# Kernel optimization log

Measured on AMD Instinct MI355X. Metric: run time of the kernel, lower is better.

Reference implementation:

```python
import jax, jax.numpy as jnp
import numpy as np

N = 50000      # nodes per graph
E = 1_600_000  # edges per graph (before self-loops)
D = 128        # node feature dim
H = 9          # attention heads
C = 8          # channels per head
HC = H * C     # 72
NEG_SLOPE = 0.2


def setup_inputs() -> dict:
    key = jax.random.key(0)
    ks = iter(jax.random.split(key, 32))
    inp = {}
    for i in (1, 2, 3):
        inp[f"x{i}"] = jax.random.normal(next(ks), (N, D), dtype=jnp.float32)
        inp[f"edge_index{i}"] = jax.random.randint(next(ks), (2, E), 0, N, dtype=jnp.int64)
        inp[f"W{i}"] = jax.random.normal(next(ks), (D, HC), dtype=jnp.float32) * (1.0 / np.sqrt(D))
        inp[f"att_src{i}"] = jax.random.normal(next(ks), (H, C), dtype=jnp.float32) * 0.1
        inp[f"att_dst{i}"] = jax.random.normal(next(ks), (H, C), dtype=jnp.float32) * 0.1
        inp[f"b{i}"] = jnp.zeros((HC,), dtype=jnp.float32)
    inp["fnn_W"] = jax.random.normal(next(ks), (3 * HC, 2), dtype=jnp.float32) * (1.0 / np.sqrt(3 * HC))
    inp["fnn_b"] = jnp.zeros((2,), dtype=jnp.float32)
    return inp


def gat_conv(x, edge_index, W, att_src, att_dst, bias):
    """PyG GATConv (eval mode): linear -> per-edge LeakyReLU score -> edge softmax
    over incoming edges per dst node -> scatter-add aggregate. Self-loops added."""
    n = x.shape[0]
    loop = jnp.arange(n, dtype=edge_index.dtype)
    src = jnp.concatenate([edge_index[0], loop])  # [E+N]
    dst = jnp.concatenate([edge_index[1], loop])
    h = (x @ W).reshape(n, H, C)                  # [N,H,C]
    a_s = jnp.einsum('nhc,hc->nh', h, att_src)    # [N,H]
    a_d = jnp.einsum('nhc,hc->nh', h, att_dst)
    alpha = jax.nn.leaky_relu(a_s[src] + a_d[dst], NEG_SLOPE)   # [E+N,H]
    m = jax.ops.segment_max(alpha, dst, num_segments=n)         # stable softmax per dst
    alpha = jnp.exp(alpha - m[dst])
    denom = jax.ops.segment_sum(alpha, dst, num_segments=n)
    alpha = alpha / (denom[dst] + 1e-16)
    out = jax.ops.segment_sum(h[src] * alpha[:, :, None], dst, num_segments=n)
    return out.reshape(n, HC) + bias


def reference(x1, x2, x3, edge_index1, edge_index2, edge_index3,
              W1, att_src1, att_dst1, b1,
              W2, att_src2, att_dst2, b2,
              W3, att_src3, att_dst3, b3,
              fnn_W, fnn_b):
    o1 = gat_conv(x1, edge_index1, W1, att_src1, att_dst1, b1)
    o2 = gat_conv(x2, edge_index2, W2, att_src2, att_dst2, b2)
    o3 = gat_conv(x3, edge_index3, W3, att_src3, att_dst3, b3)
    x = jax.nn.relu(jnp.concatenate([o1, o2, o3], axis=1))  # [N, 216]
    logits = x @ fnn_W + fnn_b                              # [N, 2]
    return jax.nn.softmax(logits, axis=1)
```

## Files before the change

kernel.cpp:

```cpp
#include <hip/hip_runtime.h>
#include <hip/hip_fp16.h>

#define NN 50000
#define NE 1600000
#define DD 128
#define NH 9
#define NC 8
#define HCH 72
#define NEG 0.2f
#define NBUCK 196
#define NSEG 16
#define SPAD 17
#define EPB 16
#define BCH (256*EPB)
#define BSTRIDE 10240
#define BCSTRIDE 16
#define GEMMB2 ((NN + 63) / 64)
#define BINB ((NE + BCH - 1) / BCH)
#define WTP 136
#define CLP 88

typedef _Float16 f16x8 __attribute__((ext_vector_type(8)));
typedef float f32x4 __attribute__((ext_vector_type(4)));

__device__ __forceinline__ unsigned short f2h(float f) {
  return __half_as_ushort(__float2half_rn(f));
}
__device__ __forceinline__ float h2f(unsigned short u) {
  return __half2float(__ushort_as_half(u));
}
__device__ __forceinline__ float hlo(unsigned u) {
  return __half2float(__ushort_as_half((unsigned short)(u & 0xFFFFu)));
}
__device__ __forceinline__ float hhi(unsigned u) {
  return __half2float(__ushort_as_half((unsigned short)(u >> 16)));
}

struct GP {
  const float* x; const int* ei; const float* W;
  const float* as; const float* ad; const float* b;
  uint4* h2;
  unsigned short* as2;
  float* a_d; float* out;
  int* offs2;
  int* bcursor;
  unsigned int* pairs;
  int* csr;
};
struct GT { GP g[3]; };

__global__ __launch_bounds__(256) void k_gemm_bin(GT t) {
  const GP G = t.g[blockIdx.z];
  __shared__ __align__(16) char smem[80 * WTP * 2 + 64 * CLP * 2];
  const int tid = threadIdx.x;

  if (blockIdx.x >= GEMMB2) {
    int* lh    = (int*)smem;
    int* lbase = lh + 256;
    int* lcur  = lbase + 256;
    const int e0 = (blockIdx.x - GEMMB2) * BCH;
    for (int i = tid; i < NBUCK; i += 256) lh[i] = 0;
    __syncthreads();
    int dsts[EPB], srcs[EPB];
    #pragma unroll
    for (int k = 0; k < EPB; ++k) {
      const int e = e0 + k * 256 + tid;
      if (e < NE) {
        dsts[k] = G.ei[NE + e];
        srcs[k] = G.ei[e];
        atomicAdd(&lh[dsts[k] >> 8], 1);
      } else dsts[k] = -1;
    }
    __syncthreads();
    for (int i = tid; i < NBUCK; i += 256) {
      int c = lh[i];
      lbase[i] = c ? atomicAdd(&G.bcursor[i * BCSTRIDE], c) : 0;
      lcur[i] = 0;
    }
    __syncthreads();
    #pragma unroll
    for (int k = 0; k < EPB; ++k) {
      if (dsts[k] >= 0) {
        int b = dsts[k] >> 8;
        int pos = lbase[b] + atomicAdd(&lcur[b], 1);
        if (pos < BSTRIDE)
          G.pairs[(size_t)b * BSTRIDE + pos] =
              (unsigned)srcs[k] | ((unsigned)(dsts[k] & 255) << 16);
      }
    }
    return;
  }

  _Float16* Wt = (_Float16*)smem;
  _Float16* Cl = (_Float16*)(smem + 80 * WTP * 2);

  for (int i = tid; i < DD * 80; i += 256) {
    const int k = i / 80;
    const int c = i - k * 80;
    const float v = (c < HCH) ? G.W[k * HCH + c] : 0.f;
    Wt[c * WTP + k] = (_Float16)v;
  }
  __syncthreads();

  const int wv = tid >> 6;
  const int ln = tid & 63;
  const int rl = ln & 15;
  const int kg = ln >> 4;
  const int n0 = blockIdx.x << 6;
  int arow = n0 + wv * 16 + rl;
  if (arow >= NN) arow = NN - 1;
  const float4* xr = (const float4*)(G.x + (size_t)arow * DD) + (kg << 1);

  f32x4 acc[5];
  #pragma unroll
  for (int ct = 0; ct < 5; ++ct) acc[ct] = (f32x4){0.f, 0.f, 0.f, 0.f};

  #pragma unroll
  for (int ks = 0; ks < 4; ++ks) {
    const float4 xa = xr[ks * 8];
    const float4 xb = xr[ks * 8 + 1];
    float xs[8] = {xa.x, xa.y, xa.z, xa.w, xb.x, xb.y, xb.z, xb.w};
    f16x8 ahi, alo;
    #pragma unroll
    for (int j = 0; j < 8; ++j) {
      const _Float16 h = (_Float16)xs[j];
      ahi[j] = h;
      alo[j] = (_Float16)(xs[j] - (float)h);
    }
    const int kb = ks * 32 + kg * 8;
    #pragma unroll
    for (int ct = 0; ct < 5; ++ct) {
      const f16x8 bf = *(const f16x8*)&Wt[(ct * 16 + rl) * WTP + kb];
      acc[ct] = __builtin_amdgcn_mfma_f32_16x16x32_f16(ahi, bf, acc[ct], 0, 0, 0);
      acc[ct] = __builtin_amdgcn_mfma_f32_16x16x32_f16(alo, bf, acc[ct], 0, 0, 0);
    }
  }

  #pragma unroll
  for (int ct = 0; ct < 5; ++ct) {
    #pragma unroll
    for (int j = 0; j < 4; ++j)
      Cl[(wv * 16 + kg * 4 + j) * CLP + ct * 16 + rl] = (_Float16)acc[ct][j];
  }
  __syncthreads();

  for (int p = tid; p < 64 * NH; p += 256) {
    const int node = p / NH;
    const int hd = p - node * NH;
    const int n = n0 + node;
    if (n >= NN) continue;
    const uint4 hv = *(const uint4*)&Cl[node * CLP + hd * NC];
    const float h0 = hlo(hv.x), h1 = hhi(hv.x), h2v = hlo(hv.y), h3 = hhi(hv.y);
    const float h4 = hlo(hv.z), h5 = hhi(hv.z), h6 = hlo(hv.w), h7 = hhi(hv.w);
    const float4 As0 = *(const float4*)(G.as + hd * NC);
    const float4 As1 = *(const float4*)(G.as + hd * NC + 4);
    const float4 Ad0 = *(const float4*)(G.ad + hd * NC);
    const float4 Ad1 = *(const float4*)(G.ad + hd * NC + 4);
    const float ssrc = h0 * As0.x + h1 * As0.y + h2v * As0.z + h3 * As0.w
                     + h4 * As1.x + h5 * As1.y + h6 * As1.z + h7 * As1.w;
    const float sdst = h0 * Ad0.x + h1 * Ad0.y + h2v * Ad0.z + h3 * Ad0.w
                     + h4 * Ad1.x + h5 * Ad1.y + h6 * Ad1.z + h7 * Ad1.w;
    G.h2[(size_t)n * NH + hd] = hv;
    G.as2[n * NH + hd] = f2h(ssrc);
    G.a_d[n * NH + hd] = sdst;
  }
}

__global__ __launch_bounds__(256) void k_scat2(GT t) {
  const GP G = t.g[blockIdx.z];
  const int b = blockIdx.x;
  const int d0 = b << 8;
  __shared__ int cnt[256 * SPAD];
  __shared__ int ssum[256];
  const int tid = threadIdx.x;
  const int estart = b * BSTRIDE;
  const int eend = estart + G.bcursor[b * BCSTRIDE];
  for (int i = tid; i < 256 * SPAD; i += 256) cnt[i] = 0;
  __syncthreads();
  for (int e = estart + tid; e < eend; e += 256) {
    unsigned p = G.pairs[e];
    int key = (int)((p >> 16) * SPAD + ((p & 0xFFFFu) >> 12));
    atomicAdd(&cnt[key], 1);
  }
  __syncthreads();
  int local[NSEG];
  int sum = 0;
  #pragma unroll
  for (int i = 0; i < NSEG; ++i) { local[i] = sum; sum += cnt[tid * SPAD + i]; }
  ssum[tid] = sum;
  __syncthreads();
  int run = sum;
  for (int off = 1; off < 256; off <<= 1) {
    int u = (tid >= off) ? ssum[tid - off] : 0;
    __syncthreads();
    run += u;
    ssum[tid] = run;
    __syncthreads();
  }
  const int texcl = run - sum;
  int* o2 = G.offs2 + ((size_t)d0 << 4);
  #pragma unroll
  for (int i = 0; i < NSEG; ++i) {
    int v = estart + texcl + local[i];
    cnt[tid * SPAD + i] = v;
    o2[tid * NSEG + i] = v;
  }
  __syncthreads();
  for (int e = estart + tid; e < eend; e += 256) {
    unsigned p = G.pairs[e];
    int key = (int)((p >> 16) * SPAD + ((p & 0xFFFFu) >> 12));
    int pos = atomicAdd(&cnt[key], 1);
    G.csr[pos] = (int)(p & 0xFFFFu);
  }
}

__global__ __launch_bounds__(256) void k_agg(GP G) {
  const int gid = blockIdx.x * 256 + threadIdx.x;
  const bool active = (gid < NN * NH);
  int n = 0, head = 0;
  if (active) { n = gid / NH; head = gid - n * NH; }
  float denom = 0.f;
  float4 acc0 = make_float4(0.f, 0.f, 0.f, 0.f);
  float4 acc1 = make_float4(0.f, 0.f, 0.f, 0.f);
  float ad_n = 0.f;
  int gb[5] = {0, 0, 0, 0, 0};
  if (active) {
    ad_n = G.a_d[n * NH + head];
    const int* o2 = G.offs2 + ((size_t)n << 4);
    gb[0] = o2[0]; gb[1] = o2[4]; gb[2] = o2[8]; gb[3] = o2[12]; gb[4] = o2[13];
    float sl = h2f(G.as2[n * NH + head]) + ad_n;
    sl = (sl > 0.f) ? sl : NEG * sl;
    float wl = __expf(sl);
    uint4 hs = G.h2[(size_t)n * NH + head];
    denom = wl;
    acc0.x = wl * hlo(hs.x); acc0.y = wl * hhi(hs.x);
    acc0.z = wl * hlo(hs.y); acc0.w = wl * hhi(hs.y);
    acc1.x = wl * hlo(hs.z); acc1.y = wl * hhi(hs.z);
    acc1.z = wl * hlo(hs.w); acc1.w = wl * hhi(hs.w);
  }
  #pragma unroll
  for (int g = 0; g < 4; ++g) {
    int e = gb[g];
    const int en = gb[g + 1];
    for (; e + 4 <= en; e += 4) {
      int s0 = G.csr[e];
      int s1 = G.csr[e + 1];
      int s2 = G.csr[e + 2];
      int s3 = G.csr[e + 3];
      unsigned short u0 = G.as2[s0 * NH + head];
      unsigned short u1 = G.as2[s1 * NH + head];
      unsigned short u2 = G.as2[s2 * NH + head];
      unsigned short u3 = G.as2[s3 * NH + head];
      uint4 v0 = G.h2[(size_t)s0 * NH + head];
      uint4 v1 = G.h2[(size_t)s1 * NH + head];
      uint4 v2 = G.h2[(size_t)s2 * NH + head];
      uint4 v3 = G.h2[(size_t)s3 * NH + head];
      float t0 = h2f(u0) + ad_n;
      float t1 = h2f(u1) + ad_n;
      float t2 = h2f(u2) + ad_n;
      float t3 = h2f(u3) + ad_n;
      t0 = (t0 > 0.f) ? t0 : NEG * t0;
      t1 = (t1 > 0.f) ? t1 : NEG * t1;
      t2 = (t2 > 0.f) ? t2 : NEG * t2;
      t3 = (t3 > 0.f) ? t3 : NEG * t3;
      float w0 = __expf(t0);
      float w1 = __expf(t1);
      float w2 = __expf(t2);
      float w3 = __expf(t3);
      denom += (w0 + w1) + (w2 + w3);
      acc0.x = fmaf(w0, hlo(v0.x), acc0.x); acc0.y = fmaf(w0, hhi(v0.x), acc0.y);
      acc0.z = fmaf(w0, hlo(v0.y), acc0.z); acc0.w = fmaf(w0, hhi(v0.y), acc0.w);
      acc1.x = fmaf(w0, hlo(v0.z), acc1.x); acc1.y = fmaf(w0, hhi(v0.z), acc1.y);
      acc1.z = fmaf(w0, hlo(v0.w), acc1.z); acc1.w = fmaf(w0, hhi(v0.w), acc1.w);
      acc0.x = fmaf(w1, hlo(v1.x), acc0.x); acc0.y = fmaf(w1, hhi(v1.x), acc0.y);
      acc0.z = fmaf(w1, hlo(v1.y), acc0.z); acc0.w = fmaf(w1, hhi(v1.y), acc0.w);
      acc1.x = fmaf(w1, hlo(v1.z), acc1.x); acc1.y = fmaf(w1, hhi(v1.z), acc1.y);
      acc1.z = fmaf(w1, hlo(v1.w), acc1.z); acc1.w = fmaf(w1, hhi(v1.w), acc1.w);
      acc0.x = fmaf(w2, hlo(v2.x), acc0.x); acc0.y = fmaf(w2, hhi(v2.x), acc0.y);
      acc0.z = fmaf(w2, hlo(v2.y), acc0.z); acc0.w = fmaf(w2, hhi(v2.y), acc0.w);
      acc1.x = fmaf(w2, hlo(v2.z), acc1.x); acc1.y = fmaf(w2, hhi(v2.z), acc1.y);
      acc1.z = fmaf(w2, hlo(v2.w), acc1.z); acc1.w = fmaf(w2, hhi(v2.w), acc1.w);
      acc0.x = fmaf(w3, hlo(v3.x), acc0.x); acc0.y = fmaf(w3, hhi(v3.x), acc0.y);
      acc0.z = fmaf(w3, hlo(v3.y), acc0.z); acc0.w = fmaf(w3, hhi(v3.y), acc0.w);
      acc1.x = fmaf(w3, hlo(v3.z), acc1.x); acc1.y = fmaf(w3, hhi(v3.z), acc1.y);
      acc1.z = fmaf(w3, hlo(v3.w), acc1.z); acc1.w = fmaf(w3, hhi(v3.w), acc1.w);
    }
    for (; e < en; ++e) {
      int src = G.csr[e];
      float sc = h2f(G.as2[src * NH + head]) + ad_n;
      sc = (sc > 0.f) ? sc : NEG * sc;
      float w = __expf(sc);
      uint4 hv = G.h2[(size_t)src * NH + head];
      denom += w;
      acc0.x = fmaf(w, hlo(hv.x), acc0.x); acc0.y = fmaf(w, hhi(hv.x), acc0.y);
      acc0.z = fmaf(w, hlo(hv.y), acc0.z); acc0.w = fmaf(w, hhi(hv.y), acc0.w);
      acc1.x = fmaf(w, hlo(hv.z), acc1.x); acc1.y = fmaf(w, hhi(hv.z), acc1.y);
      acc1.z = fmaf(w, hlo(hv.w), acc1.z); acc1.w = fmaf(w, hhi(hv.w), acc1.w);
    }
    __syncthreads();
  }
  if (!active) return;
  float inv = 1.f / (denom + 1e-16f);
  const float* bp = G.b + head * NC;
  float4 o0, o1;
  o0.x = acc0.x * inv + bp[0]; o0.y = acc0.y * inv + bp[1];
  o0.z = acc0.z * inv + bp[2]; o0.w = acc0.w * inv + bp[3];
  o1.x = acc1.x * inv + bp[4]; o1.y = acc1.y * inv + bp[5];
  o1.z = acc1.z * inv + bp[6]; o1.w = acc1.w * inv + bp[7];
  float4* op = (float4*)(G.out + (size_t)n * HCH + head * NC);
  op[0] = o0; op[1] = o1;
}

__global__ __launch_bounds__(256) void k_fnn(const float* __restrict__ o1,
                                             const float* __restrict__ o2,
                                             const float* __restrict__ o3,
                                             const float* __restrict__ fw,
                                             const float* __restrict__ fb,
                                             float* __restrict__ out) {
  const int tid = blockIdx.x * 256 + threadIdx.x;
  const int n = tid >> 6;
  const int lane = tid & 63;
  if (n >= NN) return;
  float acc0 = 0.f, acc1 = 0.f;
  for (int j = lane; j < 3 * HCH; j += 64) {
    const int g = j / HCH;
    const int c = j - g * HCH;
    const float* og = (g == 0) ? o1 : (g == 1) ? o2 : o3;
    float v = og[(size_t)n * HCH + c];
    v = v > 0.f ? v : 0.f;
    acc0 = fmaf(v, fw[2 * j], acc0);
    acc1 = fmaf(v, fw[2 * j + 1], acc1);
  }
  #pragma unroll
  for (int off = 32; off > 0; off >>= 1) {
    acc0 += __shfl_down(acc0, off, 64);
    acc1 += __shfl_down(acc1, off, 64);
  }
  if (lane == 0) {
    float l0 = acc0 + fb[0], l1 = acc1 + fb[1];
    float m = fmaxf(l0, l1);
    float e0 = __expf(l0 - m), e1 = __expf(l1 - m);
    float inv = 1.f / (e0 + e1);
    out[(size_t)n * 2] = e0 * inv;
    out[(size_t)n * 2 + 1] = e1 * inv;
  }
}

extern "C" void kernel_launch(void* const* d_in, const int* in_sizes, int n_in,
                              void* d_out, int out_size, void* d_ws, size_t ws_size,
                              hipStream_t stream) {
  (void)in_sizes; (void)n_in; (void)out_size; (void)ws_size;
  GT t;
  char* w = (char*)d_ws;
  size_t off = 0;
  auto carve = [&](size_t bytes) -> void* {
    void* p = w + off;
    off = (off + bytes + 255) & ~(size_t)255;
    return p;
  };
  int* bc_all = (int*)carve(3 * NBUCK * BCSTRIDE * 4);
  for (int g = 0; g < 3; ++g) {
    GP& G = t.g[g];
    G.x  = (const float*)d_in[6 * g + 0];
    G.ei = (const int*)d_in[6 * g + 1];
    G.W  = (const float*)d_in[6 * g + 2];
    G.as = (const float*)d_in[6 * g + 3];
    G.ad = (const float*)d_in[6 * g + 4];
    G.b  = (const float*)d_in[6 * g + 5];
    G.bcursor = bc_all + g * NBUCK * BCSTRIDE;
    G.h2   = (uint4*)carve((size_t)NN * NH * 16);
    G.as2  = (unsigned short*)carve((size_t)NN * NH * 2);
    G.a_d  = (float*)carve((size_t)NN * NH * 4);
    G.out  = (float*)carve((size_t)NN * HCH * 4);
    G.offs2 = (int*)carve((size_t)NBUCK * 256 * NSEG * 4);
    G.pairs = (unsigned int*)carve((size_t)NBUCK * BSTRIDE * 4);
    G.csr   = (int*)carve((size_t)NBUCK * BSTRIDE * 4);
  }
  const float* fw = (const float*)d_in[18];
  const float* fb = (const float*)d_in[19];
  float* outp = (float*)d_out;

  dim3 b256(256, 1, 1);
  hipMemsetAsync(bc_all, 0, 3 * NBUCK * BCSTRIDE * 4, stream);
  k_gemm_bin<<<dim3(GEMMB2 + BINB, 1, 3), b256, 0, stream>>>(t);
  k_scat2   <<<dim3(NBUCK, 1, 3), b256, 0, stream>>>(t);
  for (int g = 0; g < 3; ++g)
    k_agg   <<<dim3((NN * NH + 255) / 256, 1, 1), b256, 0, stream>>>(t.g[g]);
  k_fnn     <<<(NN * 64 + 255) / 256, b256, 0, stream>>>(t.g[0].out, t.g[1].out, t.g[2].out, fw, fb, outp);
}
```

Before: 433.1 us.

## Split binning kernel, stage pairs in LDS for coalesced writes, merge agg launches

Edge binning moves out of the fused gemm/bin kernel into its own kernel. Each block now sorts its edges into buckets locally in shared memory using a prefix scan, then writes contiguous runs to the global pairs array, replacing scattered per-edge global writes. The three per-graph aggregation launches are merged into one grid, which cuts launch overhead and tail idle time. In exchange it adds an extra kernel launch, more LDS use per binning block, and gives up the overlap between GEMM and binning that the fused kernel had.

Measured after the change: 436.8 us. About the same (+0.8%).

```diff
diff --git a/kernel.cpp b/kernel.cpp
--- a/kernel.cpp
+++ b/kernel.cpp
@@ -17,6 +17,7 @@
 #define BCSTRIDE 16
 #define GEMMB2 ((NN + 63) / 64)
 #define BINB ((NE + BCH - 1) / BCH)
+#define AGGB ((NN * NH + 255) / 256)
 #define WTP 136
 #define CLP 88
 
@@ -49,48 +50,10 @@
 };
 struct GT { GP g[3]; };
 
-__global__ __launch_bounds__(256) void k_gemm_bin(GT t) {
+__global__ __launch_bounds__(256) void k_gemm(GT t) {
   const GP G = t.g[blockIdx.z];
   __shared__ __align__(16) char smem[80 * WTP * 2 + 64 * CLP * 2];
   const int tid = threadIdx.x;
-
-  if (blockIdx.x >= GEMMB2) {
-    int* lh    = (int*)smem;
-    int* lbase = lh + 256;
-    int* lcur  = lbase + 256;
-    const int e0 = (blockIdx.x - GEMMB2) * BCH;
-    for (int i = tid; i < NBUCK; i += 256) lh[i] = 0;
-    __syncthreads();
-    int dsts[EPB], srcs[EPB];
-    #pragma unroll
-    for (int k = 0; k < EPB; ++k) {
-      const int e = e0 + k * 256 + tid;
-      if (e < NE) {
-        dsts[k] = G.ei[NE + e];
-        srcs[k] = G.ei[e];
-        atomicAdd(&lh[dsts[k] >> 8], 1);
-      } else dsts[k] = -1;
-    }
-    __syncthreads();
-    for (int i = tid; i < NBUCK; i += 256) {
-      int c = lh[i];
-      lbase[i] = c ? atomicAdd(&G.bcursor[i * BCSTRIDE], c) : 0;
-      lcur[i] = 0;
-    }
-    __syncthreads();
-    #pragma unroll
-    for (int k = 0; k < EPB; ++k) {
-      if (dsts[k] >= 0) {
-        int b = dsts[k] >> 8;
-        int pos = lbase[b] + atomicAdd(&lcur[b], 1);
-        if (pos < BSTRIDE)
-          G.pairs[(size_t)b * BSTRIDE + pos] =
-              (unsigned)srcs[k] | ((unsigned)(dsts[k] & 255) << 16);
-      }
-    }
-    return;
-  }
-
   _Float16* Wt = (_Float16*)smem;
   _Float16* Cl = (_Float16*)(smem + 80 * WTP * 2);
 
@@ -166,6 +129,66 @@
   }
 }
 
+__global__ __launch_bounds__(256) void k_bin(GT t) {
+  const GP G = t.g[blockIdx.z];
+  __shared__ unsigned stage[BCH];
+  __shared__ unsigned char bkt[BCH];
+  __shared__ int hist[NBUCK];
+  __shared__ int gdelta[NBUCK];
+  __shared__ int ssum[256];
+  const int tid = threadIdx.x;
+  const int e0 = blockIdx.x * BCH;
+
+  for (int i = tid; i < NBUCK; i += 256) hist[i] = 0;
+  __syncthreads();
+  int dsts[EPB], srcs[EPB];
+  #pragma unroll
+  for (int k = 0; k < EPB; ++k) {
+    const int e = e0 + k * 256 + tid;
+    if (e < NE) {
+      dsts[k] = G.ei[NE + e];
+      srcs[k] = G.ei[e];
+      atomicAdd(&hist[dsts[k] >> 8], 1);
+    } else dsts[k] = -1;
+  }
+  __syncthreads();
+  const int cnt_t = (tid < NBUCK) ? hist[tid] : 0;
+  ssum[tid] = cnt_t;
+  __syncthreads();
+  int run = cnt_t;
+  for (int off = 1; off < 256; off <<= 1) {
+    int u = (tid >= off) ? ssum[tid - off] : 0;
+    __syncthreads();
+    run += u;
+    ssum[tid] = run;
+    __syncthreads();
+  }
+  const int excl = run - cnt_t;
+  if (tid < NBUCK) {
+    const int gbase = cnt_t ? atomicAdd(&G.bcursor[tid * BCSTRIDE], cnt_t) : 0;
+    gdelta[tid] = tid * BSTRIDE + gbase - excl;
+    hist[tid] = excl;
+  }
+  __syncthreads();
+  #pragma unroll
+  for (int k = 0; k < EPB; ++k) {
+    if (dsts[k] >= 0) {
+      const int b = dsts[k] >> 8;
+      const int pos = atomicAdd(&hist[b], 1);
+      stage[pos] = (unsigned)srcs[k] | ((unsigned)(dsts[k] & 255) << 16);
+      bkt[pos] = (unsigned char)b;
+    }
+  }
+  __syncthreads();
+  const int total = (e0 + BCH <= NE) ? BCH : (NE - e0);
+  for (int i = tid; i < total; i += 256) {
+    const int b = bkt[i];
+    const int addr = gdelta[b] + i;
+    if (addr - b * BSTRIDE < BSTRIDE)
+      G.pairs[addr] = stage[i];
+  }
+}
+
 __global__ __launch_bounds__(256) void k_scat2(GT t) {
   const GP G = t.g[blockIdx.z];
   const int b = blockIdx.x;
@@ -214,8 +237,10 @@
   }
 }
 
-__global__ __launch_bounds__(256) void k_agg(GP G) {
-  const int gid = blockIdx.x * 256 + threadIdx.x;
+__global__ __launch_bounds__(256) void k_agg(GT t) {
+  const int g = blockIdx.x / AGGB;
+  const GP G = t.g[g];
+  const int gid = (blockIdx.x - g * AGGB) * 256 + threadIdx.x;
   const bool active = (gid < NN * NH);
   int n = 0, head = 0;
   if (active) { n = gid / NH; head = gid - n * NH; }
@@ -239,9 +264,9 @@
     acc1.z = wl * hlo(hs.w); acc1.w = wl * hhi(hs.w);
   }
   #pragma unroll
-  for (int g = 0; g < 4; ++g) {
-    int e = gb[g];
-    const int en = gb[g + 1];
+  for (int sgrp = 0; sgrp < 4; ++sgrp) {
+    int e = gb[sgrp];
+    const int en = gb[sgrp + 1];
     for (; e + 4 <= en; e += 4) {
       int s0 = G.csr[e];
       int s1 = G.csr[e + 1];
@@ -382,9 +407,9 @@
 
   dim3 b256(256, 1, 1);
   hipMemsetAsync(bc_all, 0, 3 * NBUCK * BCSTRIDE * 4, stream);
-  k_gemm_bin<<<dim3(GEMMB2 + BINB, 1, 3), b256, 0, stream>>>(t);
-  k_scat2   <<<dim3(NBUCK, 1, 3), b256, 0, stream>>>(t);
-  for (int g = 0; g < 3; ++g)
-    k_agg   <<<dim3((NN * NH + 255) / 256, 1, 1), b256, 0, stream>>>(t.g[g]);
-  k_fnn     <<<(NN * 64 + 255) / 256, b256, 0, stream>>>(t.g[0].out, t.g[1].out, t.g[2].out, fw, fb, outp);
-}
+  k_bin   <<<dim3(BINB, 1, 3), b256, 0, stream>>>(t);
+  k_gemm  <<<dim3(GEMMB2, 1, 3), b256, 0, stream>>>(t);
+  k_scat2 <<<dim3(NBUCK, 1, 3), b256, 0, stream>>>(t);
+  k_agg   <<<dim3(AGGB * 3, 1, 1), b256, 0, stream>>>(t);
+  k_fnn   <<<(NN * 64 + 255) / 256, b256, 0, stream>>>(t.g[0].out, t.g[1].out, t.g[2].out, fw, fb, outp);
+}
```
